# Optimization experiments

Hardware: AMD Instinct MI355X
Metric: run time of the kernel (lower is better)

Reference implementation:

```python
import jax, jax.numpy as jnp
import numpy as np

VOCAB = 100000
SEQ = 2048
NSYN = 4
D = 300      # embedding_size
H1 = 300     # biLSTM output dim (150 per direction)
U = 150      # LSTM units per direction


def _lstm(x, Wk, Wr, b, reverse=False):
    """Keras-style LSTM over [S, D] -> [S, U]. Gate order i, f, g(cell), o."""
    if reverse:
        x = x[::-1]
    u = Wr.shape[0]

    def step(carry, xt):
        h, c = carry
        z = xt @ Wk + h @ Wr + b              # [4U]
        i, f, g, o = jnp.split(z, 4, axis=-1)
        i = jax.nn.sigmoid(i)
        f = jax.nn.sigmoid(f)
        g = jnp.tanh(g)
        o = jax.nn.sigmoid(o)
        c = f * c + i * g
        h = o * jnp.tanh(c)
        return (h, c), h

    init = (jnp.zeros((u,), x.dtype), jnp.zeros((u,), x.dtype))
    _, hs = jax.lax.scan(step, init, x)
    return hs[::-1] if reverse else hs


def setup_inputs() -> dict:
    key = jax.random.key(0)
    ks = jax.random.split(key, 14)
    w = 0.05  # small init so exp() attention coefficients stay stable
    return {
        "sentence": jax.random.randint(ks[0], (SEQ,), 0, VOCAB),
        "synonym_indices": jax.random.randint(ks[1], (VOCAB, NSYN), 0, VOCAB),
        "embedding_matrix": jax.random.normal(ks[2], (VOCAB, D), jnp.float32) * 0.1,
        # forward LSTM
        "Wk_f": jax.random.normal(ks[3], (D, 4 * U), jnp.float32) * w,
        "Wr_f": jax.random.normal(ks[4], (U, 4 * U), jnp.float32) * w,
        "b_f": jnp.zeros((4 * U,), jnp.float32),
        # backward LSTM
        "Wk_b": jax.random.normal(ks[5], (D, 4 * U), jnp.float32) * w,
        "Wr_b": jax.random.normal(ks[6], (U, 4 * U), jnp.float32) * w,
        "b_b": jnp.zeros((4 * U,), jnp.float32),
        # primary attention dense (h1 -> h1)
        "W1": jax.random.normal(ks[7], (H1, H1), jnp.float32) * w,
        "b1": jnp.zeros((H1,), jnp.float32),
        # secondary attention dense (h1 -> 1, tanh)
        "W2": jax.random.normal(ks[8], (H1, 1), jnp.float32) * w,
        "b2": jnp.zeros((1,), jnp.float32),
        # output heads
        "We": jax.random.normal(ks[9], (H1, 8), jnp.float32) * w,
        "be": jnp.zeros((8,), jnp.float32),
        "Ws": jax.random.normal(ks[10], (H1, 1), jnp.float32) * w,
        "bs": jnp.zeros((1,), jnp.float32),
    }


def reference(sentence, synonym_indices, embedding_matrix,
              Wk_f, Wr_f, b_f, Wk_b, Wr_b, b_b,
              W1, b1, W2, b2, We, be, Ws, bs):
    emb = embedding_matrix[sentence]                       # [S, D]
    hf = _lstm(emb, Wk_f, Wr_f, b_f)                       # [S, U]
    hb = _lstm(emb, Wk_b, Wr_b, b_b, reverse=True)         # [S, U]
    hidden = jnp.concatenate([hf, hb], axis=-1)            # [S, H1]

    # ---- primary attention (vectorized over all tokens) ----
    out = hidden @ W1 + b1                                 # [S, H1]
    S = sentence.shape[0]
    # Faithful off-by-one from the original loop: token 0 uses row 0,
    # token i (i>=1) uses out/hidden row i-1.
    idx = jnp.concatenate([jnp.zeros((1,), jnp.int32),
                           jnp.arange(S - 1, dtype=jnp.int32)])
    syn_emb = embedding_matrix[synonym_indices[sentence]]  # [S, NSYN, D]
    coeff = jnp.exp(jnp.einsum('skd,sd->sk', syn_emb, out[idx]))  # [S, NSYN]
    m = jnp.einsum('sk,skd->sd', coeff, syn_emb)           # [S, D]
    h_hats = m + hidden[idx]                               # [S, H1]

    # ---- secondary attention ----
    c2 = jnp.exp(jnp.tanh(h_hats @ W2 + b2))               # [S, 1]
    H = jnp.sum(c2 * h_hats, axis=0)[None, :]              # [1, H1]

    emotion_logits = H @ We + be                           # [1, 8]
    sentiment_logits = H @ Ws + bs                         # [1, 1]
    return (emotion_logits, sentiment_logits)
```

## Files before the change

### kernel.cpp

```cpp
#include <hip/hip_runtime.h>
#include <hip/hip_bf16.h>

#define SEQ   2048
#define DIM   300
#define UU    150
#define G4    600
#define H1    300
#define NSYN  4

typedef _Float16 half2v __attribute__((ext_vector_type(2)));
typedef unsigned u32x4 __attribute__((ext_vector_type(4)));
union HU { unsigned u; half2v h; };

static __device__ __forceinline__ float sigm(float x) { return 1.0f / (1.0f + __expf(-x)); }
static __device__ __forceinline__ float tanh_fast(float x) { return 1.0f - 2.0f / (1.0f + __expf(2.0f * x)); }

static __device__ __forceinline__ float dot2v(unsigned w, unsigned h, float acc) {
    asm("v_dot2_f32_f16 %0, %1, %2, %0" : "+v"(acc) : "v"(w), "v"(h));
    return acc;
}

#define LDS_BARRIER() asm volatile("s_waitcnt lgkmcnt(0)\n\ts_barrier" ::: "memory")

__global__ void xpre_kernel(const int* __restrict__ sentence,
                            const float* __restrict__ emb_mat,
                            const float* __restrict__ Wk_f,
                            const float* __restrict__ b_f,
                            const float* __restrict__ Wk_b,
                            const float* __restrict__ b_b,
                            float* __restrict__ Xf, float* __restrict__ Xb)
{
    const int dir = blockIdx.y;
    const float* Wk = dir ? Wk_b : Wk_f;
    const float* bb = dir ? b_b : b_f;
    float* X = dir ? Xb : Xf;

    const int s0  = blockIdx.x * 8;
    const int tid = threadIdx.x;

    __shared__ int   sids[8];
    __shared__ float embs[8][DIM];

    if (tid < 8) sids[tid] = sentence[s0 + tid];
    __syncthreads();
    for (int e = tid; e < 8 * DIM; e += 640) {
        int r = e / DIM, d = e - r * DIM;
        embs[r][d] = emb_mat[(long)sids[r] * DIM + d];
    }
    __syncthreads();

    if (tid < G4) {
        float acc[8];
        float bv = bb[tid];
        #pragma unroll
        for (int r = 0; r < 8; ++r) acc[r] = bv;
        for (int k = 0; k < DIM; ++k) {
            float wv = Wk[k * G4 + tid];
            #pragma unroll
            for (int r = 0; r < 8; ++r) acc[r] = fmaf(embs[r][k], wv, acc[r]);
        }
        #pragma unroll
        for (int r = 0; r < 8; ++r) X[(long)(s0 + r) * G4 + tid] = acc[r];
    }
}

#define REP76(F) \
  F(0) F(1) F(2) F(3) F(4) F(5) F(6) F(7) F(8) F(9) \
  F(10) F(11) F(12) F(13) F(14) F(15) F(16) F(17) F(18) F(19) \
  F(20) F(21) F(22) F(23) F(24) F(25) F(26) F(27) F(28) F(29) \
  F(30) F(31) F(32) F(33) F(34) F(35) F(36) F(37) F(38) F(39) \
  F(40) F(41) F(42) F(43) F(44) F(45) F(46) F(47) F(48) F(49) \
  F(50) F(51) F(52) F(53) F(54) F(55) F(56) F(57) F(58) F(59) \
  F(60) F(61) F(62) F(63) F(64) F(65) F(66) F(67) F(68) F(69) \
  F(70) F(71) F(72) F(73) F(74) F(75)

static __device__ __forceinline__ unsigned packpair2(const float* __restrict__ Wr, int c, int k) {
    if (k >= 75) return 0u;
    HU x;
    x.h.x = (_Float16)Wr[(2 * k) * G4 + c];
    x.h.y = (_Float16)Wr[(2 * k + 1) * G4 + c];
    return x.u;
}

__global__ __launch_bounds__(320) __attribute__((amdgpu_waves_per_eu(2, 2)))
void lstm_scan_kernel(
    const float* __restrict__ Xf, const float* __restrict__ Xb,
    const float* __restrict__ Wr_f, const float* __restrict__ Wr_b,
    float* __restrict__ hidden)
{
    const int dir = blockIdx.x;
    const float* X  = dir ? Xb : Xf;
    const float* Wr = dir ? Wr_b : Wr_f;
    const int tid  = threadIdx.x;
    const int l    = tid & 63;
    const int w    = tid >> 6;
    const int isB  = l >> 5;
    const int j    = (w << 5) + (l & 31);
    const bool active = (j < UU);
    const int u    = active ? j : (UU - 1);
    const int cA   = u + isB * UU;
    const int cB   = cA + 300;

    __shared__ __align__(16) unsigned hsbuf[2][80];

#define WDECL(k) unsigned wA_##k, wB_##k;
    REP76(WDECL)
#undef WDECL
#define WLOAD(k) wA_##k = packpair2(Wr, cA, k); wB_##k = packpair2(Wr, cB, k);
    REP76(WLOAD)
#undef WLOAD

    for (int e = tid; e < 160; e += 320) ((unsigned*)hsbuf)[e] = 0u;

    float c = 0.0f;
    int tt = dir ? (SEQ - 1) : 0;
    const int dt = dir ? -1 : 1;
    float xA = X[(long)tt * G4 + cA];
    float xB = X[(long)tt * G4 + cB];
    float* hout = hidden + dir * UU + u;
    __syncthreads();

    for (int step = 0; step < SEQ; ++step) {
        const int tn = (step < SEQ - 1) ? (tt + dt) : tt;
        float xAn = X[(long)tn * G4 + cA];
        float xBn = X[(long)tn * G4 + cB];

        const u32x4* hb = (const u32x4*)hsbuf[step & 1];
        u32x4 h0 = hb[0], h1 = hb[1], h2 = hb[2], h3 = hb[3], h4 = hb[4];
        u32x4 h5 = hb[5], h6 = hb[6], h7 = hb[7], h8 = hb[8], h9 = hb[9];

        float a0a = xA, a0b = 0.0f, a1a = xB, a1b = 0.0f;

#define DOTQ(k0,k1,k2,k3,hv) \
        a0a = dot2v(wA_##k0, hv.x, a0a); a1a = dot2v(wB_##k0, hv.x, a1a); \
        a0b = dot2v(wA_##k1, hv.y, a0b); a1b = dot2v(wB_##k1, hv.y, a1b); \
        a0a = dot2v(wA_##k2, hv.z, a0a); a1a = dot2v(wB_##k2, hv.z, a1a); \
        a0b = dot2v(wA_##k3, hv.w, a0b); a1b = dot2v(wB_##k3, hv.w, a1b);

        DOTQ(0,1,2,3,h0)     DOTQ(4,5,6,7,h1)     DOTQ(8,9,10,11,h2)
        DOTQ(12,13,14,15,h3) DOTQ(16,17,18,19,h4)
        h0 = hb[10]; h1 = hb[11]; h2 = hb[12]; h3 = hb[13]; h4 = hb[14];
        DOTQ(20,21,22,23,h5) DOTQ(24,25,26,27,h6) DOTQ(28,29,30,31,h7)
        DOTQ(32,33,34,35,h8) DOTQ(36,37,38,39,h9)
        h5 = hb[15]; h6 = hb[16]; h7 = hb[17]; h8 = hb[18];
        DOTQ(40,41,42,43,h0) DOTQ(44,45,46,47,h1) DOTQ(48,49,50,51,h2)
        DOTQ(52,53,54,55,h3) DOTQ(56,57,58,59,h4)
        DOTQ(60,61,62,63,h5) DOTQ(64,65,66,67,h6) DOTQ(68,69,70,71,h7)
        DOTQ(72,73,74,75,h8)
#undef DOTQ

        const float a0 = a0a + a0b;
        const float a1 = a1a + a1b;

        float s0 = sigm(a0);
        float t1 = tanh_fast(a1);
        float s1 = sigm(a1);
        float ig = s0 * t1;
        float igx = __shfl_xor(ig, 32);
        c = s0 * c + igx;
        float th = tanh_fast(c);
        float hv = s1 * th;

        if (isB && active) {
            ((_Float16*)hsbuf[(step & 1) ^ 1])[u] = (_Float16)hv;
            hout[(long)tt * H1] = hv;
        }
        LDS_BARRIER();

        xA = xAn; xB = xBn; tt = tn;
    }
}

__global__ void w1_kernel(const float* __restrict__ hidden,
                          const float* __restrict__ W1,
                          const float* __restrict__ b1,
                          float* __restrict__ outm)
{
    const int s0  = blockIdx.x * 8;
    const int tid = threadIdx.x;
    __shared__ float hl[8][H1];
    for (int e = tid; e < 8 * H1; e += 320)
        hl[e / H1][e - (e / H1) * H1] = hidden[(long)s0 * H1 + e];
    __syncthreads();

    if (tid < H1) {
        float acc[8];
        float bv = b1[tid];
        #pragma unroll
        for (int r = 0; r < 8; ++r) acc[r] = bv;
        for (int k = 0; k < H1; ++k) {
            float wv = W1[k * H1 + tid];
            #pragma unroll
            for (int r = 0; r < 8; ++r) acc[r] = fmaf(hl[r][k], wv, acc[r]);
        }
        #pragma unroll
        for (int r = 0; r < 8; ++r) outm[(long)(s0 + r) * H1 + tid] = acc[r];
    }
}

static __device__ __forceinline__ float4 blockReduce4(float4 v, float* red, int tid)
{
    #pragma unroll
    for (int off = 32; off > 0; off >>= 1) {
        v.x += __shfl_down(v.x, off);
        v.y += __shfl_down(v.y, off);
        v.z += __shfl_down(v.z, off);
        v.w += __shfl_down(v.w, off);
    }
    __syncthreads();
    if ((tid & 63) == 0) {
        int wv = tid >> 6;
        red[wv * 4 + 0] = v.x; red[wv * 4 + 1] = v.y;
        red[wv * 4 + 2] = v.z; red[wv * 4 + 3] = v.w;
    }
    __syncthreads();
    float4 r;
    r.x = red[0]; r.y = red[1]; r.z = red[2]; r.w = red[3];
    #pragma unroll
    for (int wv = 1; wv < 5; ++wv) {
        r.x += red[wv * 4 + 0]; r.y += red[wv * 4 + 1];
        r.z += red[wv * 4 + 2]; r.w += red[wv * 4 + 3];
    }
    return r;
}

static __device__ __forceinline__ float blockReduce1(float v, float* red, int tid)
{
    #pragma unroll
    for (int off = 32; off > 0; off >>= 1) v += __shfl_down(v, off);
    __syncthreads();
    if ((tid & 63) == 0) red[tid >> 6] = v;
    __syncthreads();
    return red[0] + red[1] + red[2] + red[3] + red[4];
}

__global__ void attn_kernel(const int* __restrict__ sentence,
                            const int* __restrict__ syn_idx,
                            const float* __restrict__ emb_mat,
                            const float* __restrict__ outm,
                            const float* __restrict__ hidden,
                            const float* __restrict__ W2,
                            const float* __restrict__ b2,
                            float* __restrict__ whh)
{
    const int s   = blockIdx.x;
    const int t   = s ? (s - 1) : 0;
    const int tid = threadIdx.x;
    __shared__ float red[20];

    const int sent = sentence[s];
    const long i0 = (long)syn_idx[sent * NSYN + 0] * DIM;
    const long i1 = (long)syn_idx[sent * NSYN + 1] * DIM;
    const long i2 = (long)syn_idx[sent * NSYN + 2] * DIM;
    const long i3 = (long)syn_idx[sent * NSYN + 3] * DIM;

    float se0 = 0.f, se1 = 0.f, se2 = 0.f, se3 = 0.f, od = 0.f, hd = 0.f;
    if (tid < DIM) {
        se0 = emb_mat[i0 + tid];
        se1 = emb_mat[i1 + tid];
        se2 = emb_mat[i2 + tid];
        se3 = emb_mat[i3 + tid];
        od  = outm[(long)t * H1 + tid];
        hd  = hidden[(long)t * H1 + tid];
    }

    float4 dots = blockReduce4(make_float4(se0 * od, se1 * od, se2 * od, se3 * od), red, tid);
    float c0 = __expf(dots.x), c1 = __expf(dots.y), c2c = __expf(dots.z), c3 = __expf(dots.w);

    float hh = fmaf(c0, se0, fmaf(c1, se1, fmaf(c2c, se2, fmaf(c3, se3, hd))));

    float w2v = (tid < DIM) ? W2[tid] : 0.f;
    float dot2 = blockReduce1(hh * w2v, red, tid);
    float cc = __expf(tanh_fast(dot2 + b2[0]));

    if (tid < DIM) whh[(long)s * H1 + tid] = cc * hh;
}

__global__ void hred_kernel(const float* __restrict__ whh, float* __restrict__ H)
{
    const int d   = blockIdx.x;
    const int tid = threadIdx.x;
    float acc = 0.f;
    for (int s = tid; s < SEQ; s += 256) acc += whh[(long)s * H1 + d];
    #pragma unroll
    for (int off = 32; off > 0; off >>= 1) acc += __shfl_down(acc, off);
    __shared__ float red[4];
    if ((tid & 63) == 0) red[tid >> 6] = acc;
    __syncthreads();
    if (tid == 0) H[d] = red[0] + red[1] + red[2] + red[3];
}

__global__ void logits_kernel(const float* __restrict__ H,
                              const float* __restrict__ We,
                              const float* __restrict__ be,
                              const float* __restrict__ Ws,
                              const float* __restrict__ bs,
                              float* __restrict__ outp)
{
    const int e = threadIdx.x;
    if (e < 9) {
        float acc = (e < 8) ? be[e] : bs[0];
        for (int d = 0; d < H1; ++d) {
            float wv = (e < 8) ? We[d * 8 + e] : Ws[d];
            acc = fmaf(H[d], wv, acc);
        }
        outp[e] = acc;
    }
}

extern "C" void kernel_launch(void* const* d_in, const int* in_sizes, int n_in,
                              void* d_out, int out_size, void* d_ws, size_t ws_size,
                              hipStream_t stream)
{
    const int* sentence   = (const int*)d_in[0];
    const int* syn_idx    = (const int*)d_in[1];
    const float* emb      = (const float*)d_in[2];
    const float* Wk_f     = (const float*)d_in[3];
    const float* Wr_f     = (const float*)d_in[4];
    const float* b_f      = (const float*)d_in[5];
    const float* Wk_b     = (const float*)d_in[6];
    const float* Wr_b     = (const float*)d_in[7];
    const float* b_b      = (const float*)d_in[8];
    const float* W1       = (const float*)d_in[9];
    const float* b1       = (const float*)d_in[10];
    const float* W2       = (const float*)d_in[11];
    const float* b2       = (const float*)d_in[12];
    const float* We       = (const float*)d_in[13];
    const float* be       = (const float*)d_in[14];
    const float* Ws       = (const float*)d_in[15];
    const float* bs       = (const float*)d_in[16];

    float* ws     = (float*)d_ws;
    float* Xf     = ws;
    float* Xb     = Xf + (long)SEQ * G4;
    float* hidden = Xb + (long)SEQ * G4;
    float* outm   = hidden + (long)SEQ * H1;
    float* whh    = outm + (long)SEQ * H1;
    float* H      = whh + (long)SEQ * H1;

    float* outp = (float*)d_out;

    xpre_kernel<<<dim3(SEQ / 8, 2), 640, 0, stream>>>(sentence, emb, Wk_f, b_f, Wk_b, b_b, Xf, Xb);
    lstm_scan_kernel<<<2, 320, 0, stream>>>(Xf, Xb, Wr_f, Wr_b, hidden);
    w1_kernel<<<SEQ / 8, 320, 0, stream>>>(hidden, W1, b1, outm);
    attn_kernel<<<SEQ, 320, 0, stream>>>(sentence, syn_idx, emb, outm, hidden, W2, b2, whh);
    hred_kernel<<<H1, 256, 0, stream>>>(whh, H);
    logits_kernel<<<1, 64, 0, stream>>>(H, We, be, Ws, bs, outp);
}
```

Baseline: 2.513 ms.

## Split LSTM recurrence across four threads per unit, one gate column each

The LSTM scan kernel goes from 320 to 640 threads. Each thread now holds the packed fp16 recurrent weights for a single gate column, where before it held two. Gate activations are combined across the four threads of a unit with two xor-shuffles, and the forget-gate thread updates the cell and writes h. This halves the serial dot2 chain per thread on the latency-bound recurrence, at the cost of twice as many waves at each per-step barrier and extra cross-lane shuffles.

```diff
diff --git a/kernel.cpp b/kernel.cpp
--- a/kernel.cpp
+++ b/kernel.cpp
@@ -82,7 +82,7 @@
     return x.u;
 }
 
-__global__ __launch_bounds__(320) __attribute__((amdgpu_waves_per_eu(2, 2)))
+__global__ __launch_bounds__(640)
 void lstm_scan_kernel(
     const float* __restrict__ Xf, const float* __restrict__ Xb,
     const float* __restrict__ Wr_f, const float* __restrict__ Wr_b,
@@ -91,83 +91,77 @@
     const int dir = blockIdx.x;
     const float* X  = dir ? Xb : Xf;
     const float* Wr = dir ? Wr_b : Wr_f;
-    const int tid  = threadIdx.x;
-    const int l    = tid & 63;
-    const int w    = tid >> 6;
-    const int isB  = l >> 5;
-    const int j    = (w << 5) + (l & 31);
-    const bool active = (j < UU);
-    const int u    = active ? j : (UU - 1);
-    const int cA   = u + isB * UU;
-    const int cB   = cA + 300;
+    const int tid = threadIdx.x;
+    const int g   = tid & 3;
+    const int q   = tid >> 2;
+    const bool active = (q < UU);
+    const int u   = active ? q : (UU - 1);
+    const int col = g * UU + u;
 
     __shared__ __align__(16) unsigned hsbuf[2][80];
 
-#define WDECL(k) unsigned wA_##k, wB_##k;
+#define WDECL(k) unsigned w_##k;
     REP76(WDECL)
 #undef WDECL
-#define WLOAD(k) wA_##k = packpair2(Wr, cA, k); wB_##k = packpair2(Wr, cB, k);
+#define WLOAD(k) w_##k = packpair2(Wr, col, k);
     REP76(WLOAD)
 #undef WLOAD
 
-    for (int e = tid; e < 160; e += 320) ((unsigned*)hsbuf)[e] = 0u;
+    for (int e = tid; e < 160; e += 640) ((unsigned*)hsbuf)[e] = 0u;
 
     float c = 0.0f;
     int tt = dir ? (SEQ - 1) : 0;
     const int dt = dir ? -1 : 1;
-    float xA = X[(long)tt * G4 + cA];
-    float xB = X[(long)tt * G4 + cB];
+    float x = X[(long)tt * G4 + col];
+    const bool writer = (g == 1) && active;
     float* hout = hidden + dir * UU + u;
     __syncthreads();
 
     for (int step = 0; step < SEQ; ++step) {
         const int tn = (step < SEQ - 1) ? (tt + dt) : tt;
-        float xAn = X[(long)tn * G4 + cA];
-        float xBn = X[(long)tn * G4 + cB];
+        float xn = X[(long)tn * G4 + col];
 
         const u32x4* hb = (const u32x4*)hsbuf[step & 1];
         u32x4 h0 = hb[0], h1 = hb[1], h2 = hb[2], h3 = hb[3], h4 = hb[4];
-        u32x4 h5 = hb[5], h6 = hb[6], h7 = hb[7], h8 = hb[8], h9 = hb[9];
-
-        float a0a = xA, a0b = 0.0f, a1a = xB, a1b = 0.0f;
+
+        float aa = x, ab = 0.0f;
 
 #define DOTQ(k0,k1,k2,k3,hv) \
-        a0a = dot2v(wA_##k0, hv.x, a0a); a1a = dot2v(wB_##k0, hv.x, a1a); \
-        a0b = dot2v(wA_##k1, hv.y, a0b); a1b = dot2v(wB_##k1, hv.y, a1b); \
-        a0a = dot2v(wA_##k2, hv.z, a0a); a1a = dot2v(wB_##k2, hv.z, a1a); \
-        a0b = dot2v(wA_##k3, hv.w, a0b); a1b = dot2v(wB_##k3, hv.w, a1b);
+        aa = dot2v(w_##k0, hv.x, aa); ab = dot2v(w_##k1, hv.y, ab); \
+        aa = dot2v(w_##k2, hv.z, aa); ab = dot2v(w_##k3, hv.w, ab);
 
         DOTQ(0,1,2,3,h0)     DOTQ(4,5,6,7,h1)     DOTQ(8,9,10,11,h2)
         DOTQ(12,13,14,15,h3) DOTQ(16,17,18,19,h4)
+        h0 = hb[5]; h1 = hb[6]; h2 = hb[7]; h3 = hb[8]; h4 = hb[9];
+        DOTQ(20,21,22,23,h0) DOTQ(24,25,26,27,h1) DOTQ(28,29,30,31,h2)
+        DOTQ(32,33,34,35,h3) DOTQ(36,37,38,39,h4)
         h0 = hb[10]; h1 = hb[11]; h2 = hb[12]; h3 = hb[13]; h4 = hb[14];
-        DOTQ(20,21,22,23,h5) DOTQ(24,25,26,27,h6) DOTQ(28,29,30,31,h7)
-        DOTQ(32,33,34,35,h8) DOTQ(36,37,38,39,h9)
-        h5 = hb[15]; h6 = hb[16]; h7 = hb[17]; h8 = hb[18];
         DOTQ(40,41,42,43,h0) DOTQ(44,45,46,47,h1) DOTQ(48,49,50,51,h2)
         DOTQ(52,53,54,55,h3) DOTQ(56,57,58,59,h4)
-        DOTQ(60,61,62,63,h5) DOTQ(64,65,66,67,h6) DOTQ(68,69,70,71,h7)
-        DOTQ(72,73,74,75,h8)
+        h0 = hb[15]; h1 = hb[16]; h2 = hb[17]; h3 = hb[18];
+        DOTQ(60,61,62,63,h0) DOTQ(64,65,66,67,h1) DOTQ(68,69,70,71,h2)
+        DOTQ(72,73,74,75,h3)
 #undef DOTQ
 
-        const float a0 = a0a + a0b;
-        const float a1 = a1a + a1b;
-
-        float s0 = sigm(a0);
-        float t1 = tanh_fast(a1);
-        float s1 = sigm(a1);
-        float ig = s0 * t1;
-        float igx = __shfl_xor(ig, 32);
-        c = s0 * c + igx;
+        const float z = aa + ab;
+
+        float s  = sigm(z);
+        float tz = tanh_fast(z);
+        float act  = (g == 2) ? tz : s;
+        float act2 = __shfl_xor(act, 2);
+        float p    = act * act2;
+        float px   = __shfl_xor(p, 1);
+        c = s * c + px;
         float th = tanh_fast(c);
-        float hv = s1 * th;
-
-        if (isB && active) {
+        float hv = act2 * th;
+
+        if (writer) {
             ((_Float16*)hsbuf[(step & 1) ^ 1])[u] = (_Float16)hv;
             hout[(long)tt * H1] = hv;
         }
         LDS_BARRIER();
 
-        xA = xAn; xB = xBn; tt = tn;
+        x = xn; tt = tn;
     }
 }
 
@@ -341,7 +335,7 @@
     float* outp = (float*)d_out;
 
     xpre_kernel<<<dim3(SEQ / 8, 2), 640, 0, stream>>>(sentence, emb, Wk_f, b_f, Wk_b, b_b, Xf, Xb);
-    lstm_scan_kernel<<<2, 320, 0, stream>>>(Xf, Xb, Wr_f, Wr_b, hidden);
+    lstm_scan_kernel<<<2, 640, 0, stream>>>(Xf, Xb, Wr_f, Wr_b, hidden);
     w1_kernel<<<SEQ / 8, 320, 0, stream>>>(hidden, W1, b1, outm);
     attn_kernel<<<SEQ, 320, 0, stream>>>(sentence, syn_idx, emb, outm, hidden, W2, b2, whh);
     hred_kernel<<<H1, 256, 0, stream>>>(whh, H);
```

New measurement: 2.428 ms. -3.4%, faster.
